# Kernel optimization log

Hardware: AMD Instinct MI355X
Metric: run time of the kernel (lower is better)

Reference implementation:

```python
import jax, jax.numpy as jnp
import numpy as np

B, T, I, H = 256, 2048, 128, 128


def setup_inputs() -> dict:
    key = jax.random.key(0)
    ks = jax.random.split(key, 6)
    x = jax.random.normal(ks[0], (B, T, I), dtype=jnp.float32)
    lengths = jax.random.randint(ks[1], (B,), 1, T + 1)  # pack_padded requires >=1
    s = 1.0 / np.sqrt(H)  # PyTorch LSTM init range
    W_ih = jax.random.uniform(ks[2], (4 * H, I), minval=-s, maxval=s, dtype=jnp.float32)
    W_hh = jax.random.uniform(ks[3], (4 * H, H), minval=-s, maxval=s, dtype=jnp.float32)
    b_ih = jax.random.uniform(ks[4], (4 * H,), minval=-s, maxval=s, dtype=jnp.float32)
    b_hh = jax.random.uniform(ks[5], (4 * H,), minval=-s, maxval=s, dtype=jnp.float32)
    return {"x": x, "lengths": lengths, "W_ih": W_ih, "W_hh": W_hh, "b_ih": b_ih, "b_hh": b_hh}


def reference(x, lengths, W_ih, W_hh, b_ih, b_hh):
    # Single-layer batch_first LSTM over a packed (variable-length) batch.
    # PyTorch gate order: i, f, g, o.  State frozen once t >= length.
    Bn, Tn, _ = x.shape
    Hn = W_hh.shape[1]
    # Precompute the input projection for all timesteps (one big GEMM): [B,T,4H]
    x_proj = jnp.einsum('bti,gi->btg', x, W_ih) + b_ih + b_hh
    x_proj = jnp.moveaxis(x_proj, 1, 0)  # [T,B,4H] for scan over time
    tgrid = jnp.arange(Tn)

    def step(carry, inp):
        h, c = carry
        xp, t = inp
        gates = xp + h @ W_hh.T  # [B,4H]
        i, f, g, o = jnp.split(gates, 4, axis=-1)
        i = jax.nn.sigmoid(i)
        f = jax.nn.sigmoid(f)
        o = jax.nn.sigmoid(o)
        g = jnp.tanh(g)
        c_new = f * c + i * g
        h_new = o * jnp.tanh(c_new)
        valid = (t < lengths)[:, None]
        h = jnp.where(valid, h_new, h)
        c = jnp.where(valid, c_new, c)
        return (h, c), None

    h0 = jnp.zeros((Bn, Hn), x.dtype)
    (h, _), _ = jax.lax.scan(step, (h0, h0), (x_proj, tgrid))
    # pad_packed_sequence zero-pads: output at index T-1 is h_{T-1} only for
    # full-length sequences, zeros otherwise.
    return jnp.where((lengths == Tn)[:, None], h, jnp.zeros_like(h))
```

## Files before the change

### kernel.cpp

```cpp
#include <hip/hip_runtime.h>
#include <math.h>

#define BB 256
#define TT 2048
#define II 128
#define HH 128
#define GG 512
#define SLOT_FLOATS (TT * GG)
#define TC 16

__device__ __forceinline__ float sigmoidf_(float v) {
    return 1.0f / (1.0f + expf(-v));
}

__global__ __launch_bounds__(GG, 2) void xproj_kernel(
    const float* __restrict__ x, const int* __restrict__ lengths,
    const float* __restrict__ W_ih, const float* __restrict__ b_ih,
    const float* __restrict__ b_hh, float* __restrict__ ws, int slots)
{
    const int b = blockIdx.x;
    if (lengths[b] != TT) return;
    int rank = 0;
    for (int k = 0; k < b; ++k) rank += (lengths[k] == TT);
    if (rank >= slots) return;

    const int g  = threadIdx.x;
    const int t0 = blockIdx.y * 64;

    __shared__ float xs[64][II];
    const float4* xin = (const float4*)(x + ((size_t)b * TT + t0) * II);
    float4* xs4 = (float4*)&xs[0][0];
    for (int idx = g; idx < 64 * II / 4; idx += GG) xs4[idx] = xin[idx];
    __syncthreads();

    float4 wr[32];
    const float4* wrow = (const float4*)(W_ih + (size_t)g * II);
#pragma unroll
    for (int i = 0; i < 32; ++i) wr[i] = wrow[i];

    const float bias = b_ih[g] + b_hh[g];
    float* outp = ws + (size_t)rank * SLOT_FLOATS + (size_t)t0 * GG + g;

    for (int t = 0; t < 64; ++t) {
        float acc = bias;
        const float4* xr = (const float4*)&xs[t][0];
#pragma unroll
        for (int i = 0; i < 32; ++i) {
            float4 xv = xr[i];
            acc += wr[i].x * xv.x + wr[i].y * xv.y + wr[i].z * xv.z + wr[i].w * xv.w;
        }
        outp[(size_t)t * GG] = acc;
    }
}

__global__ __launch_bounds__(GG, 2) void lstm_kernel(
    const float* __restrict__ x, const int* __restrict__ lengths,
    const float* __restrict__ W_ih, const float* __restrict__ W_hh,
    const float* __restrict__ b_ih, const float* __restrict__ b_hh,
    const float* __restrict__ ws, int slots, float* __restrict__ out)
{
    const int b = blockIdx.x;
    const int g = threadIdx.x;
    const int len = lengths[b];
    if (len != TT) {
        if (g < HH) out[b * HH + g] = 0.0f;
        return;
    }

    int rank = 0;
    for (int k = 0; k < b; ++k) rank += (lengths[k] == TT);
    const bool use_ws = (rank < slots);

    __shared__ float h_lds[HH];
    __shared__ float gates_lds[GG];
    __shared__ float xs[TC][II];

    float4 wh[32];
    const float4* whrow = (const float4*)(W_hh + (size_t)g * HH);
#pragma unroll
    for (int i = 0; i < 32; ++i) wh[i] = whrow[i];

    const float4* wirow = (const float4*)(W_ih + (size_t)g * II);
    const float bias = b_ih[g] + b_hh[g];
    const float* xp_base = ws + (size_t)rank * SLOT_FLOATS + g;

    float c = 0.0f;
    if (g < HH) h_lds[g] = 0.0f;
    __syncthreads();

    for (int t = 0; t < TT; ++t) {
        float acc;
        if (use_ws) {
            acc = xp_base[(size_t)t * GG];
        } else {
            if ((t & (TC - 1)) == 0) {
                const float4* xin = (const float4*)(x + ((size_t)b * TT + t) * II);
                float4* xs4 = (float4*)&xs[0][0];
                for (int idx = g; idx < TC * II / 4; idx += GG) xs4[idx] = xin[idx];
                __syncthreads();
            }
            acc = bias;
            const float4* xr = (const float4*)&xs[t & (TC - 1)][0];
#pragma unroll
            for (int i = 0; i < 32; ++i) {
                float4 wv = wirow[i];
                float4 xv = xr[i];
                acc += wv.x * xv.x + wv.y * xv.y + wv.z * xv.z + wv.w * xv.w;
            }
        }

        const float4* hr = (const float4*)&h_lds[0];
#pragma unroll
        for (int i = 0; i < 32; ++i) {
            float4 hv = hr[i];
            acc += wh[i].x * hv.x + wh[i].y * hv.y + wh[i].z * hv.z + wh[i].w * hv.w;
        }
        gates_lds[g] = acc;
        __syncthreads();

        if (g < HH) {
            float iv = sigmoidf_(gates_lds[g]);
            float fv = sigmoidf_(gates_lds[HH + g]);
            float gv = tanhf(gates_lds[2 * HH + g]);
            float ov = sigmoidf_(gates_lds[3 * HH + g]);
            c = fv * c + iv * gv;
            h_lds[g] = ov * tanhf(c);
        }
        __syncthreads();
    }

    if (g < HH) out[b * HH + g] = h_lds[g];
}

extern "C" void kernel_launch(void* const* d_in, const int* in_sizes, int n_in,
                              void* d_out, int out_size, void* d_ws, size_t ws_size,
                              hipStream_t stream) {
    const float* x       = (const float*)d_in[0];
    const int*   lengths = (const int*)d_in[1];
    const float* W_ih    = (const float*)d_in[2];
    const float* W_hh    = (const float*)d_in[3];
    const float* b_ih    = (const float*)d_in[4];
    const float* b_hh    = (const float*)d_in[5];
    float* out = (float*)d_out;
    float* ws  = (float*)d_ws;

    const size_t slot_bytes = (size_t)SLOT_FLOATS * sizeof(float);
    int slots = (int)(ws_size / slot_bytes);
    if (slots > 8) slots = 8;

    if (slots > 0) {
        hipLaunchKernelGGL(xproj_kernel, dim3(BB, TT / 64), dim3(GG), 0, stream,
                           x, lengths, W_ih, b_ih, b_hh, ws, slots);
    }
    hipLaunchKernelGGL(lstm_kernel, dim3(BB), dim3(GG), 0, stream,
                       x, lengths, W_ih, W_hh, b_ih, b_hh, ws, slots, out);
}
```

Measured before the change: 301.8 us.

## Fuse input projection into LSTM kernel with per-block workspace prologue

Removes the separate xproj kernel launch and instead has each full-length sequence block compute its own input projection into a workspace slot indexed by batch index, before running the recurrence. The slot cap rises from 8 to the batch size, so more sequences take the precomputed path instead of recomputing W_ih·x inside the serial loop. This trades the parallel multi-block projection for a serial per-block prologue, and it drops the unroll on the fallback W_ih loop. It also increases register pressure from holding both weight sets.

```diff
diff --git a/kernel.cpp b/kernel.cpp
--- a/kernel.cpp
+++ b/kernel.cpp
@@ -13,76 +13,60 @@
     return 1.0f / (1.0f + expf(-v));
 }
 
-__global__ __launch_bounds__(GG, 2) void xproj_kernel(
-    const float* __restrict__ x, const int* __restrict__ lengths,
-    const float* __restrict__ W_ih, const float* __restrict__ b_ih,
-    const float* __restrict__ b_hh, float* __restrict__ ws, int slots)
-{
-    const int b = blockIdx.x;
-    if (lengths[b] != TT) return;
-    int rank = 0;
-    for (int k = 0; k < b; ++k) rank += (lengths[k] == TT);
-    if (rank >= slots) return;
-
-    const int g  = threadIdx.x;
-    const int t0 = blockIdx.y * 64;
-
-    __shared__ float xs[64][II];
-    const float4* xin = (const float4*)(x + ((size_t)b * TT + t0) * II);
-    float4* xs4 = (float4*)&xs[0][0];
-    for (int idx = g; idx < 64 * II / 4; idx += GG) xs4[idx] = xin[idx];
-    __syncthreads();
-
-    float4 wr[32];
-    const float4* wrow = (const float4*)(W_ih + (size_t)g * II);
-#pragma unroll
-    for (int i = 0; i < 32; ++i) wr[i] = wrow[i];
-
-    const float bias = b_ih[g] + b_hh[g];
-    float* outp = ws + (size_t)rank * SLOT_FLOATS + (size_t)t0 * GG + g;
-
-    for (int t = 0; t < 64; ++t) {
-        float acc = bias;
-        const float4* xr = (const float4*)&xs[t][0];
-#pragma unroll
-        for (int i = 0; i < 32; ++i) {
-            float4 xv = xr[i];
-            acc += wr[i].x * xv.x + wr[i].y * xv.y + wr[i].z * xv.z + wr[i].w * xv.w;
-        }
-        outp[(size_t)t * GG] = acc;
-    }
-}
-
-__global__ __launch_bounds__(GG, 2) void lstm_kernel(
+__global__ __launch_bounds__(GG, 2) void lstm_fused(
     const float* __restrict__ x, const int* __restrict__ lengths,
     const float* __restrict__ W_ih, const float* __restrict__ W_hh,
     const float* __restrict__ b_ih, const float* __restrict__ b_hh,
-    const float* __restrict__ ws, int slots, float* __restrict__ out)
+    float* __restrict__ ws, int slots, float* __restrict__ out)
 {
     const int b = blockIdx.x;
     const int g = threadIdx.x;
-    const int len = lengths[b];
-    if (len != TT) {
+
+    if (lengths[b] != TT) {
         if (g < HH) out[b * HH + g] = 0.0f;
         return;
     }
 
-    int rank = 0;
-    for (int k = 0; k < b; ++k) rank += (lengths[k] == TT);
-    const bool use_ws = (rank < slots);
-
+    const bool use_ws = (b < slots);
+    __shared__ float xs[TC][II];
     __shared__ float h_lds[HH];
     __shared__ float gates_lds[GG];
-    __shared__ float xs[TC][II];
+
+    const float bias = b_ih[g] + b_hh[g];
+    const float4* wirow = (const float4*)(W_ih + (size_t)g * II);
+
+    if (use_ws) {
+        float4 wi[32];
+#pragma unroll
+        for (int i = 0; i < 32; ++i) wi[i] = wirow[i];
+
+        float* xp_out = ws + (size_t)b * SLOT_FLOATS + g;
+        for (int t0 = 0; t0 < TT; t0 += TC) {
+            __syncthreads();
+            const float4* xin = (const float4*)(x + ((size_t)b * TT + t0) * II);
+            ((float4*)&xs[0][0])[g] = xin[g];
+            __syncthreads();
+#pragma unroll 4
+            for (int tt = 0; tt < TC; ++tt) {
+                float dot = 0.0f;
+                const float4* xr = (const float4*)&xs[tt][0];
+#pragma unroll
+                for (int i = 0; i < 32; ++i) {
+                    float4 xv = xr[i];
+                    dot += wi[i].x * xv.x + wi[i].y * xv.y
+                         + wi[i].z * xv.z + wi[i].w * xv.w;
+                }
+                xp_out[(size_t)(t0 + tt) * GG] = bias + dot;
+            }
+        }
+    }
 
     float4 wh[32];
     const float4* whrow = (const float4*)(W_hh + (size_t)g * HH);
 #pragma unroll
     for (int i = 0; i < 32; ++i) wh[i] = whrow[i];
 
-    const float4* wirow = (const float4*)(W_ih + (size_t)g * II);
-    const float bias = b_ih[g] + b_hh[g];
-    const float* xp_base = ws + (size_t)rank * SLOT_FLOATS + g;
+    const float* xp_in = ws + (size_t)b * SLOT_FLOATS + g;
 
     float c = 0.0f;
     if (g < HH) h_lds[g] = 0.0f;
@@ -91,30 +75,39 @@
     for (int t = 0; t < TT; ++t) {
         float acc;
         if (use_ws) {
-            acc = xp_base[(size_t)t * GG];
+            float xp = xp_in[(size_t)t * GG];
+            float dot = 0.0f;
+            const float4* hr = (const float4*)&h_lds[0];
+#pragma unroll
+            for (int i = 0; i < 32; ++i) {
+                float4 hv = hr[i];
+                dot += wh[i].x * hv.x + wh[i].y * hv.y
+                     + wh[i].z * hv.z + wh[i].w * hv.w;
+            }
+            acc = xp + dot;
         } else {
             if ((t & (TC - 1)) == 0) {
+                __syncthreads();
                 const float4* xin = (const float4*)(x + ((size_t)b * TT + t) * II);
-                float4* xs4 = (float4*)&xs[0][0];
-                for (int idx = g; idx < TC * II / 4; idx += GG) xs4[idx] = xin[idx];
+                ((float4*)&xs[0][0])[g] = xin[g];
                 __syncthreads();
             }
             acc = bias;
             const float4* xr = (const float4*)&xs[t & (TC - 1)][0];
-#pragma unroll
             for (int i = 0; i < 32; ++i) {
                 float4 wv = wirow[i];
                 float4 xv = xr[i];
                 acc += wv.x * xv.x + wv.y * xv.y + wv.z * xv.z + wv.w * xv.w;
             }
+            const float4* hr = (const float4*)&h_lds[0];
+#pragma unroll
+            for (int i = 0; i < 32; ++i) {
+                float4 hv = hr[i];
+                acc += wh[i].x * hv.x + wh[i].y * hv.y
+                     + wh[i].z * hv.z + wh[i].w * hv.w;
+            }
         }
 
-        const float4* hr = (const float4*)&h_lds[0];
-#pragma unroll
-        for (int i = 0; i < 32; ++i) {
-            float4 hv = hr[i];
-            acc += wh[i].x * hv.x + wh[i].y * hv.y + wh[i].z * hv.z + wh[i].w * hv.w;
-        }
         gates_lds[g] = acc;
         __syncthreads();
 
@@ -144,14 +137,9 @@
     float* out = (float*)d_out;
     float* ws  = (float*)d_ws;
 
-    const size_t slot_bytes = (size_t)SLOT_FLOATS * sizeof(float);
-    int slots = (int)(ws_size / slot_bytes);
-    if (slots > 8) slots = 8;
+    int slots = (int)(ws_size / ((size_t)SLOT_FLOATS * sizeof(float)));
+    if (slots > BB) slots = BB;
 
-    if (slots > 0) {
-        hipLaunchKernelGGL(xproj_kernel, dim3(BB, TT / 64), dim3(GG), 0, stream,
-                           x, lengths, W_ih, b_ih, b_hh, ws, slots);
-    }
-    hipLaunchKernelGGL(lstm_kernel, dim3(BB), dim3(GG), 0, stream,
+    hipLaunchKernelGGL(lstm_fused, dim3(BB), dim3(GG), 0, stream,
                        x, lengths, W_ih, W_hh, b_ih, b_hh, ws, slots, out);
 }
```

After: 296.5 us. No clear change (-1.8%).
